# Performance work log

Measured on AMD Instinct MI355X. Metric: run time of the kernel, lower is better.

## Reference

```python
import jax, jax.numpy as jnp
import numpy as np

B, S, D = 4, 2048, 1024


def setup_inputs() -> dict:
    key = jax.random.key(0)
    ks = jax.random.split(key, 7)
    s = 1.0 / np.sqrt(D)
    return {
        "x": jax.random.normal(ks[0], (B, S, D), dtype=jnp.float32),
        "Wq": jax.random.normal(ks[1], (D, D), dtype=jnp.float32) * s,
        "bq": jnp.zeros((D,), dtype=jnp.float32),
        "Wk": jax.random.normal(ks[2], (D, D), dtype=jnp.float32) * s,
        "bk": jnp.zeros((D,), dtype=jnp.float32),
        "Wv": jax.random.normal(ks[3], (D, D), dtype=jnp.float32) * s,
        "bv": jnp.zeros((D,), dtype=jnp.float32),
    }


def reference(x, Wq, bq, Wk, bk, Wv, bv):
    # Linear layers: x @ W^T + b (torch nn.Linear convention)
    Q = jnp.einsum("bsd,ed->bse", x, Wq) + bq
    K = jnp.einsum("bsd,ed->bse", x, Wk) + bk
    V = jnp.einsum("bsd,ed->bse", x, Wv) + bv
    scale = 1.0 / (x.shape[-1] ** 0.5)
    scores = jnp.einsum("bse,bte->bst", Q, K) * scale  # [B, S, S]
    attn = jax.nn.softmax(scores, axis=-1)
    out = jnp.einsum("bst,bte->bse", attn, V)
    return out
```

## Files before the change

kernel.cpp:

```cpp
#include <hip/hip_runtime.h>
#include <math.h>


typedef _Float16 f16;
typedef _Float16 f16x8 __attribute__((ext_vector_type(8)));
typedef _Float16 f16x4 __attribute__((ext_vector_type(4)));
typedef float f32x4 __attribute__((ext_vector_type(4)));

__device__ __forceinline__ void glds16(const void* g, const void* l) {
    __builtin_amdgcn_global_load_lds(
        (const __attribute__((address_space(1))) void*)g,
        (__attribute__((address_space(3))) void*)l, 16, 0, 0);
}

__global__ __launch_bounds__(256) void cvt16_kernel(
    const float* __restrict__ in, f16* __restrict__ o, int n4)
{
    int i = blockIdx.x * 256 + threadIdx.x;
    if (i >= n4) return;
    float4 v = ((const float4*)in)[i];
    f16x4 h = { (f16)v.x, (f16)v.y, (f16)v.z, (f16)v.w };
    ((f16x4*)o)[i] = h;
}

__global__ __launch_bounds__(256) void cvtw_kernel(
    const float* __restrict__ Wq, const float* __restrict__ Wk,
    const float* __restrict__ Wv, f16* __restrict__ o, int n4)
{
    int i = blockIdx.x * 256 + threadIdx.x;
    if (i >= n4) return;
    const float* src = (blockIdx.y == 0) ? Wq : (blockIdx.y == 1) ? Wk : Wv;
    float4 v = ((const float4*)src)[i];
    f16x4 h = { (f16)v.x, (f16)v.y, (f16)v.z, (f16)v.w };
    ((f16x4*)(o + (size_t)blockIdx.y * 1024 * 1024))[i] = h;
}

__global__ __launch_bounds__(256) void zero_kernel(float* __restrict__ p, int n)
{
    int i = blockIdx.x * 256 + threadIdx.x;
    if (i < n) p[i] = 0.0f;
}

__device__ __forceinline__ void mfma_core(
    const f16* __restrict__ A, int lda,
    const f16* __restrict__ B, int ldb,
    int K, int m0, int n0, f16* sm, f32x4 acc[4][4])
{
    f16* sA = sm;
    f16* sB = sm + 8192;

    const int tid  = threadIdx.x;
    const int lane = tid & 63;
    const int wave = tid >> 6;
    const int wm = (wave >> 1) * 64;
    const int wn = (wave & 1) * 64;
    const int lr = lane & 15;
    const int kq = lane >> 4;

    const int srow  = wave * 32;
    const int rloc  = lane >> 3;
    const int chunk = (lane & 7) ^ rloc;
    const int gcol  = chunk * 8;

    const f16* gA = A + (size_t)(m0 + srow + rloc) * lda + gcol;
    const f16* gB = B + (size_t)(n0 + srow + rloc) * ldb + gcol;

    f16* lA = sA + srow * 64;
    f16* lB = sB + srow * 64;

    for (int k0 = 0; k0 < K; k0 += 64) {
        #pragma unroll
        for (int p = 0; p < 4; ++p) {
            glds16(gA + k0 + (size_t)(p * 8) * lda, lA + p * 512);
            glds16(gB + k0 + (size_t)(p * 8) * ldb, lB + p * 512);
        }
        __syncthreads();

        #pragma unroll
        for (int kk = 0; kk < 2; ++kk) {
            f16x8 a[4], b[4];
            #pragma unroll
            for (int i = 0; i < 4; ++i) {
                const int ra = wm + i * 16 + lr;
                const int rb = wn + i * 16 + lr;
                const int c  = kk * 4 + kq;
                a[i] = *(const f16x8*)&sA[ra * 64 + ((c ^ (ra & 7)) * 8)];
                b[i] = *(const f16x8*)&sB[rb * 64 + ((c ^ (rb & 7)) * 8)];
            }
            #pragma unroll
            for (int i = 0; i < 4; ++i)
                #pragma unroll
                for (int j = 0; j < 4; ++j)
                    acc[i][j] = __builtin_amdgcn_mfma_f32_16x16x32_f16(a[i], b[j], acc[i][j], 0, 0, 0);
        }
        __syncthreads();
    }
}

__global__ __launch_bounds__(256) void qkv_mfma_kernel(
    const f16* __restrict__ xh, const f16* __restrict__ Wh,
    const float* __restrict__ bq, const float* __restrict__ bk,
    const float* __restrict__ bv,
    f16* __restrict__ Qh, f16* __restrict__ Kh, f16* __restrict__ Vh)
{
    __shared__ __align__(16) f16 smem[16384];
    const int z  = blockIdx.z;
    const int m0 = blockIdx.y * 128;
    const int n0 = blockIdx.x * 128;

    f32x4 acc[4][4];
    #pragma unroll
    for (int i = 0; i < 4; ++i)
        #pragma unroll
        for (int j = 0; j < 4; ++j) acc[i][j] = (f32x4){0.f, 0.f, 0.f, 0.f};

    mfma_core(xh, 1024, Wh + (size_t)z * 1024 * 1024, 1024, 1024, m0, n0, smem, acc);

    const float* bias = (z == 0) ? bq : (z == 1) ? bk : bv;
    const float  sc   = (z == 0) ? 0.03125f : 1.0f;
    f16* C = (z == 0) ? Qh : (z == 1) ? Kh : Vh;
    const int lane = threadIdx.x & 63;
    const int wave = threadIdx.x >> 6;
    const int wm = (wave >> 1) * 64;
    const int wn = (wave & 1) * 64;
    const int col  = lane & 15;
    const int quad = lane >> 4;

    #pragma unroll
    for (int j = 0; j < 4; ++j) {
        const int gn = n0 + wn + j * 16 + col;
        const float bb = bias[gn];
        #pragma unroll
        for (int i = 0; i < 4; ++i)
            #pragma unroll
            for (int r = 0; r < 4; ++r) {
                const int gm = m0 + wm + i * 16 + quad * 4 + r;
                C[(size_t)gm * 1024 + gn] = (f16)((acc[i][j][r] + bb) * sc);
            }
    }
}

__global__ __launch_bounds__(256) void vtrans_kernel(
    const f16* __restrict__ V, f16* __restrict__ Vt)
{
    __shared__ f16 t[64][72];
    const int b  = blockIdx.z;
    const int s0 = blockIdx.x * 64;
    const int d0 = blockIdx.y * 64;
    const int tid = threadIdx.x;

    const int r  = tid >> 3;
    const int c8 = (tid & 7) * 8;
    const f16* src = V + ((size_t)b * 2048 + s0) * 1024 + d0;
    *(f16x8*)&t[r][c8]      = *(const f16x8*)(src + (size_t)r * 1024 + c8);
    *(f16x8*)&t[r + 32][c8] = *(const f16x8*)(src + (size_t)(r + 32) * 1024 + c8);
    __syncthreads();

    const int dl  = tid >> 2;
    const int sl0 = (tid & 3) * 16;
    f16* dst = Vt + ((size_t)b * 1024 + d0 + dl) * 2048 + s0 + sl0;
    f16 buf[16];
    #pragma unroll
    for (int u = 0; u < 16; ++u) buf[u] = t[sl0 + u][dl];
    *(f16x8*)dst       = *(f16x8*)&buf[0];
    *(f16x8*)(dst + 8) = *(f16x8*)&buf[8];
}

__global__ __launch_bounds__(256) void scores_exp_kernel(
    const f16* __restrict__ Qh, const f16* __restrict__ Kh,
    f16* __restrict__ P, float* __restrict__ sums)
{
    __shared__ __align__(16) f16 smem[16384];
    const int b  = blockIdx.z;
    const int m0 = blockIdx.y * 128;
    const int n0 = blockIdx.x * 128;

    f32x4 acc[4][4];
    #pragma unroll
    for (int i = 0; i < 4; ++i)
        #pragma unroll
        for (int j = 0; j < 4; ++j) acc[i][j] = (f32x4){0.f, 0.f, 0.f, 0.f};

    const size_t ao = (size_t)b * 2048 * 1024;
    mfma_core(Qh + ao, 1024, Kh + ao, 1024, 1024, m0, n0, smem, acc);

    const int lane = threadIdx.x & 63;
    const int wave = threadIdx.x >> 6;
    const int wm = (wave >> 1) * 64;
    const int wn = (wave & 1) * 64;
    const int col  = lane & 15;
    const int quad = lane >> 4;
    f16* C = P + (size_t)b * 2048 * 2048;

    float rp[4][4];
    #pragma unroll
    for (int i = 0; i < 4; ++i)
        #pragma unroll
        for (int r = 0; r < 4; ++r) rp[i][r] = 0.0f;

    #pragma unroll
    for (int i = 0; i < 4; ++i)
        #pragma unroll
        for (int r = 0; r < 4; ++r) {
            const int gm = m0 + wm + i * 16 + quad * 4 + r;
            #pragma unroll
            for (int j = 0; j < 4; ++j) {
                const int gn = n0 + wn + j * 16 + col;
                const f16 p = (f16)__expf(acc[i][j][r]);
                C[(size_t)gm * 2048 + gn] = p;
                rp[i][r] += (float)p;
            }
        }

    #pragma unroll
    for (int i = 0; i < 4; ++i)
        #pragma unroll
        for (int r = 0; r < 4; ++r) {
            float v = rp[i][r];
            v += __shfl_xor(v, 1);
            v += __shfl_xor(v, 2);
            v += __shfl_xor(v, 4);
            v += __shfl_xor(v, 8);
            rp[i][r] = v;
        }
    if (col == 0) {
        #pragma unroll
        for (int i = 0; i < 4; ++i)
            #pragma unroll
            for (int r = 0; r < 4; ++r) {
                const int row = m0 + wm + i * 16 + quad * 4 + r;
                atomicAdd(&sums[b * 2048 + row], rp[i][r]);
            }
    }
}

__global__ __launch_bounds__(256) void pv_mfma_kernel(
    const f16* __restrict__ P, const f16* __restrict__ Vt,
    const float* __restrict__ sums, float* __restrict__ out)
{
    __shared__ __align__(16) f16 smem[16384];
    const int b  = blockIdx.z;
    const int m0 = blockIdx.y * 128;
    const int n0 = blockIdx.x * 128;

    f32x4 acc[4][4];
    #pragma unroll
    for (int i = 0; i < 4; ++i)
        #pragma unroll
        for (int j = 0; j < 4; ++j) acc[i][j] = (f32x4){0.f, 0.f, 0.f, 0.f};

    const size_t ao = (size_t)b * 2048 * 2048;
    const size_t bo = (size_t)b * 1024 * 2048;
    mfma_core(P + ao, 2048, Vt + bo, 2048, 2048, m0, n0, smem, acc);

    const int lane = threadIdx.x & 63;
    const int wave = threadIdx.x >> 6;
    const int wm = (wave >> 1) * 64;
    const int wn = (wave & 1) * 64;
    const int col  = lane & 15;
    const int quad = lane >> 4;
    float* C = out + (size_t)b * 2048 * 1024;

    #pragma unroll
    for (int i = 0; i < 4; ++i)
        #pragma unroll
        for (int r = 0; r < 4; ++r) {
            const int rl = m0 + wm + i * 16 + quad * 4 + r;
            const float inv = 1.0f / sums[b * 2048 + rl];
            #pragma unroll
            for (int j = 0; j < 4; ++j) {
                const int gn = n0 + wn + j * 16 + col;
                C[(size_t)rl * 1024 + gn] = acc[i][j][r] * inv;
            }
        }
}

extern "C" void kernel_launch(void* const* d_in, const int* in_sizes, int n_in,
                              void* d_out, int out_size, void* d_ws, size_t ws_size,
                              hipStream_t stream)
{
    (void)in_sizes; (void)n_in; (void)out_size; (void)ws_size;
    const int Bn = 4, S = 2048, D = 1024;
    const float* x  = (const float*)d_in[0];
    const float* Wq = (const float*)d_in[1];
    const float* bq = (const float*)d_in[2];
    const float* Wk = (const float*)d_in[3];
    const float* bk = (const float*)d_in[4];
    const float* Wv = (const float*)d_in[5];
    const float* bv = (const float*)d_in[6];
    float* out = (float*)d_out;

    const size_t MB = 1024 * 1024;
    char* w = (char*)d_ws;
    f16*   xh   = (f16*)(w + 0 * MB);
    f16*   Wh3  = (f16*)(w + 16 * MB);
    f16*   Vh   = (f16*)(w + 22 * MB);
    f16*   Qh   = (f16*)(w + 38 * MB);
    f16*   Kh   = (f16*)(w + 54 * MB);
    f16*   Vt   = (f16*)(w + 70 * MB);
    float* sums = (float*)(w + 86 * MB);
    f16*   P    = (f16*)(w + 0 * MB);

    cvt16_kernel<<<dim3(Bn * S * D / 4 / 256), 256, 0, stream>>>(x, xh, Bn * S * D / 4);
    cvtw_kernel<<<dim3(D * D / 4 / 256, 3), 256, 0, stream>>>(Wq, Wk, Wv, Wh3, D * D / 4);
    zero_kernel<<<dim3((Bn * S + 255) / 256), 256, 0, stream>>>(sums, Bn * S);

    qkv_mfma_kernel<<<dim3(D / 128, (Bn * S) / 128, 3), 256, 0, stream>>>(
        xh, Wh3, bq, bk, bv, Qh, Kh, Vh);
    vtrans_kernel<<<dim3(S / 64, D / 64, Bn), 256, 0, stream>>>(Vh, Vt);

    scores_exp_kernel<<<dim3(S / 128, S / 128, Bn), 256, 0, stream>>>(
        Qh, Kh, P, sums);
    pv_mfma_kernel<<<dim3(D / 128, S / 128, Bn), 256, 0, stream>>>(
        P, Vt, sums, out);
}
```

Baseline: 272.3 us.

## Triple-buffer GEMM core with 256x128 tiles, 8 waves, and grid swizzle

Replaces the single-buffered shared-memory GEMM mainloop with a three-stage async global-to-LDS pipeline using explicit vmcnt waits and raw barriers, so tile loads overlap MFMA work. Block tiles grow to 256x128 with 512 threads (8 waves), using 144KB of dynamic LDS, and the QKV projection grid is remapped with a block-index swizzle to improve cache locality. Adds setprio around the MFMA bursts. Risks lower occupancy from the large LDS footprint and fragile hand-tuned waitcnt counts.

```diff
diff --git a/kernel.cpp b/kernel.cpp
--- a/kernel.cpp
+++ b/kernel.cpp
@@ -41,72 +41,110 @@
     if (i < n) p[i] = 0.0f;
 }
 
-__device__ __forceinline__ void mfma_core(
+#define ABUF 16384
+#define BBUF 8192
+#define BOFF 49152
+
+__device__ __forceinline__ void mfma_core3(
     const f16* __restrict__ A, int lda,
     const f16* __restrict__ B, int ldb,
     int K, int m0, int n0, f16* sm, f32x4 acc[4][4])
 {
-    f16* sA = sm;
-    f16* sB = sm + 8192;
-
     const int tid  = threadIdx.x;
     const int lane = tid & 63;
-    const int wave = tid >> 6;
-    const int wm = (wave >> 1) * 64;
-    const int wn = (wave & 1) * 64;
-    const int lr = lane & 15;
-    const int kq = lane >> 4;
-
-    const int srow  = wave * 32;
-    const int rloc  = lane >> 3;
-    const int chunk = (lane & 7) ^ rloc;
-    const int gcol  = chunk * 8;
-
-    const f16* gA = A + (size_t)(m0 + srow + rloc) * lda + gcol;
-    const f16* gB = B + (size_t)(n0 + srow + rloc) * ldb + gcol;
-
-    f16* lA = sA + srow * 64;
-    f16* lB = sB + srow * 64;
-
-    for (int k0 = 0; k0 < K; k0 += 64) {
-        #pragma unroll
-        for (int p = 0; p < 4; ++p) {
-            glds16(gA + k0 + (size_t)(p * 8) * lda, lA + p * 512);
-            glds16(gB + k0 + (size_t)(p * 8) * ldb, lB + p * 512);
-        }
-        __syncthreads();
-
+    const int w    = tid >> 6;
+    const int wr   = w >> 1;
+    const int wc   = w & 1;
+    const int lr   = lane & 15;
+    const int kq   = lane >> 4;
+
+    const int rl = lane >> 3;
+    const int ch = (lane & 7) ^ rl;
+
+    const f16* gA[4];
+    #pragma unroll
+    for (int p = 0; p < 4; ++p)
+        gA[p] = A + (size_t)(m0 + p * 64 + w * 8 + rl) * lda + ch * 8;
+    const f16* gB[2];
+    #pragma unroll
+    for (int p = 0; p < 2; ++p)
+        gB[p] = B + (size_t)(n0 + p * 64 + w * 8 + rl) * ldb + ch * 8;
+
+    const int NT = K >> 6;
+
+    #pragma unroll
+    for (int s = 0; s < 2; ++s) {
+        f16* lA = sm + s * ABUF + w * 8 * 64;
+        f16* lB = sm + BOFF + s * BBUF + w * 8 * 64;
+        #pragma unroll
+        for (int p = 0; p < 4; ++p) glds16(gA[p] + s * 64, lA + p * 4096);
+        #pragma unroll
+        for (int p = 0; p < 2; ++p) glds16(gB[p] + s * 64, lB + p * 4096);
+    }
+
+    int kst = 128, sb = 2, cur = 0;
+    for (int t = 0; t < NT; ++t) {
+        if (t + 2 < NT) {
+            f16* lA = sm + sb * ABUF + w * 8 * 64;
+            f16* lB = sm + BOFF + sb * BBUF + w * 8 * 64;
+            #pragma unroll
+            for (int p = 0; p < 4; ++p) glds16(gA[p] + kst, lA + p * 4096);
+            #pragma unroll
+            for (int p = 0; p < 2; ++p) glds16(gB[p] + kst, lB + p * 4096);
+            kst += 64;
+            sb = (sb == 2) ? 0 : sb + 1;
+        }
+        if (t + 2 < NT)      asm volatile("s_waitcnt vmcnt(12)" ::: "memory");
+        else if (t + 1 < NT) asm volatile("s_waitcnt vmcnt(6)"  ::: "memory");
+        else                 asm volatile("s_waitcnt vmcnt(0)"  ::: "memory");
+        asm volatile("s_barrier" ::: "memory");
+
+        const f16* sA = sm + cur * ABUF;
+        const f16* sB = sm + BOFF + cur * BBUF;
         #pragma unroll
         for (int kk = 0; kk < 2; ++kk) {
             f16x8 a[4], b[4];
+            const int c = kk * 4 + kq;
             #pragma unroll
             for (int i = 0; i < 4; ++i) {
-                const int ra = wm + i * 16 + lr;
-                const int rb = wn + i * 16 + lr;
-                const int c  = kk * 4 + kq;
-                a[i] = *(const f16x8*)&sA[ra * 64 + ((c ^ (ra & 7)) * 8)];
-                b[i] = *(const f16x8*)&sB[rb * 64 + ((c ^ (rb & 7)) * 8)];
-            }
+                const int ar = wr * 64 + i * 16 + lr;
+                a[i] = *(const f16x8*)&sA[ar * 64 + ((c ^ (ar & 7)) * 8)];
+            }
+            #pragma unroll
+            for (int j = 0; j < 4; ++j) {
+                const int br = wc * 64 + j * 16 + lr;
+                b[j] = *(const f16x8*)&sB[br * 64 + ((c ^ (br & 7)) * 8)];
+            }
+            asm volatile("s_waitcnt lgkmcnt(0)" ::: "memory");
+            __builtin_amdgcn_sched_barrier(0);
+            __builtin_amdgcn_s_setprio(1);
             #pragma unroll
             for (int i = 0; i < 4; ++i)
                 #pragma unroll
                 for (int j = 0; j < 4; ++j)
                     acc[i][j] = __builtin_amdgcn_mfma_f32_16x16x32_f16(a[i], b[j], acc[i][j], 0, 0, 0);
-        }
-        __syncthreads();
-    }
-}
-
-__global__ __launch_bounds__(256) void qkv_mfma_kernel(
+            __builtin_amdgcn_s_setprio(0);
+            asm volatile("s_barrier" ::: "memory");
+        }
+        cur = (cur == 2) ? 0 : cur + 1;
+    }
+}
+
+__global__ __launch_bounds__(512) void qkv_mfma_kernel(
     const f16* __restrict__ xh, const f16* __restrict__ Wh,
     const float* __restrict__ bq, const float* __restrict__ bk,
     const float* __restrict__ bv,
     f16* __restrict__ Qh, f16* __restrict__ Kh, f16* __restrict__ Vh)
 {
-    __shared__ __align__(16) f16 smem[16384];
-    const int z  = blockIdx.z;
-    const int m0 = blockIdx.y * 128;
-    const int n0 = blockIdx.x * 128;
+    extern __shared__ __align__(16) f16 smem[];
+    int flat = blockIdx.x + 8 * (blockIdx.y + 32 * blockIdx.z);
+    flat = (flat & 7) * 96 + (flat >> 3);
+    const int bx = flat & 7;
+    const int by = (flat >> 3) & 31;
+    const int bz = flat >> 8;
+
+    const int m0 = by * 256;
+    const int n0 = bx * 128;
 
     f32x4 acc[4][4];
     #pragma unroll
@@ -114,27 +152,26 @@
         #pragma unroll
         for (int j = 0; j < 4; ++j) acc[i][j] = (f32x4){0.f, 0.f, 0.f, 0.f};
 
-    mfma_core(xh, 1024, Wh + (size_t)z * 1024 * 1024, 1024, 1024, m0, n0, smem, acc);
-
-    const float* bias = (z == 0) ? bq : (z == 1) ? bk : bv;
-    const float  sc   = (z == 0) ? 0.03125f : 1.0f;
-    f16* C = (z == 0) ? Qh : (z == 1) ? Kh : Vh;
+    mfma_core3(xh, 1024, Wh + (size_t)bz * 1024 * 1024, 1024, 1024, m0, n0, smem, acc);
+
+    const float* bias = (bz == 0) ? bq : (bz == 1) ? bk : bv;
+    const float  sc   = (bz == 0) ? 0.03125f : 1.0f;
+    f16* C = (bz == 0) ? Qh : (bz == 1) ? Kh : Vh;
     const int lane = threadIdx.x & 63;
-    const int wave = threadIdx.x >> 6;
-    const int wm = (wave >> 1) * 64;
-    const int wn = (wave & 1) * 64;
+    const int w    = threadIdx.x >> 6;
+    const int wr = w >> 1, wc = w & 1;
     const int col  = lane & 15;
     const int quad = lane >> 4;
 
     #pragma unroll
     for (int j = 0; j < 4; ++j) {
-        const int gn = n0 + wn + j * 16 + col;
+        const int gn = n0 + wc * 64 + j * 16 + col;
         const float bb = bias[gn];
         #pragma unroll
         for (int i = 0; i < 4; ++i)
             #pragma unroll
             for (int r = 0; r < 4; ++r) {
-                const int gm = m0 + wm + i * 16 + quad * 4 + r;
+                const int gm = m0 + wr * 64 + i * 16 + quad * 4 + r;
                 C[(size_t)gm * 1024 + gn] = (f16)((acc[i][j][r] + bb) * sc);
             }
     }
@@ -166,13 +203,13 @@
     *(f16x8*)(dst + 8) = *(f16x8*)&buf[8];
 }
 
-__global__ __launch_bounds__(256) void scores_exp_kernel(
+__global__ __launch_bounds__(512) void scores_exp_kernel(
     const f16* __restrict__ Qh, const f16* __restrict__ Kh,
     f16* __restrict__ P, float* __restrict__ sums)
 {
-    __shared__ __align__(16) f16 smem[16384];
+    extern __shared__ __align__(16) f16 smem[];
     const int b  = blockIdx.z;
-    const int m0 = blockIdx.y * 128;
+    const int m0 = blockIdx.y * 256;
     const int n0 = blockIdx.x * 128;
 
     f32x4 acc[4][4];
@@ -182,12 +219,11 @@
         for (int j = 0; j < 4; ++j) acc[i][j] = (f32x4){0.f, 0.f, 0.f, 0.f};
 
     const size_t ao = (size_t)b * 2048 * 1024;
-    mfma_core(Qh + ao, 1024, Kh + ao, 1024, 1024, m0, n0, smem, acc);
+    mfma_core3(Qh + ao, 1024, Kh + ao, 1024, 1024, m0, n0, smem, acc);
 
     const int lane = threadIdx.x & 63;
-    const int wave = threadIdx.x >> 6;
-    const int wm = (wave >> 1) * 64;
-    const int wn = (wave & 1) * 64;
+    const int w    = threadIdx.x >> 6;
+    const int wr = w >> 1, wc = w & 1;
     const int col  = lane & 15;
     const int quad = lane >> 4;
     f16* C = P + (size_t)b * 2048 * 2048;
@@ -202,10 +238,10 @@
     for (int i = 0; i < 4; ++i)
         #pragma unroll
         for (int r = 0; r < 4; ++r) {
-            const int gm = m0 + wm + i * 16 + quad * 4 + r;
+            const int gm = m0 + wr * 64 + i * 16 + quad * 4 + r;
             #pragma unroll
             for (int j = 0; j < 4; ++j) {
-                const int gn = n0 + wn + j * 16 + col;
+                const int gn = n0 + wc * 64 + j * 16 + col;
                 const f16 p = (f16)__expf(acc[i][j][r]);
                 C[(size_t)gm * 2048 + gn] = p;
                 rp[i][r] += (float)p;
@@ -228,19 +264,19 @@
         for (int i = 0; i < 4; ++i)
             #pragma unroll
             for (int r = 0; r < 4; ++r) {
-                const int row = m0 + wm + i * 16 + quad * 4 + r;
+                const int row = m0 + wr * 64 + i * 16 + quad * 4 + r;
                 atomicAdd(&sums[b * 2048 + row], rp[i][r]);
             }
     }
 }
 
-__global__ __launch_bounds__(256) void pv_mfma_kernel(
+__global__ __launch_bounds__(512) void pv_mfma_kernel(
     const f16* __restrict__ P, const f16* __restrict__ Vt,
     const float* __restrict__ sums, float* __restrict__ out)
 {
-    __shared__ __align__(16) f16 smem[16384];
+    extern __shared__ __align__(16) f16 smem[];
     const int b  = blockIdx.z;
-    const int m0 = blockIdx.y * 128;
+    const int m0 = blockIdx.y * 256;
     const int n0 = blockIdx.x * 128;
 
     f32x4 acc[4][4];
@@ -251,12 +287,11 @@
 
     const size_t ao = (size_t)b * 2048 * 2048;
     const size_t bo = (size_t)b * 1024 * 2048;
-    mfma_core(P + ao, 2048, Vt + bo, 2048, 2048, m0, n0, smem, acc);
+    mfma_core3(P + ao, 2048, Vt + bo, 2048, 2048, m0, n0, smem, acc);
 
     const int lane = threadIdx.x & 63;
-    const int wave = threadIdx.x >> 6;
-    const int wm = (wave >> 1) * 64;
-    const int wn = (wave & 1) * 64;
+    const int w    = threadIdx.x >> 6;
+    const int wr = w >> 1, wc = w & 1;
     const int col  = lane & 15;
     const int quad = lane >> 4;
     float* C = out + (size_t)b * 2048 * 1024;
@@ -265,12 +300,12 @@
     for (int i = 0; i < 4; ++i)
         #pragma unroll
         for (int r = 0; r < 4; ++r) {
-            const int rl = m0 + wm + i * 16 + quad * 4 + r;
-            const float inv = 1.0f / sums[b * 2048 + rl];
+            const int rowg = m0 + wr * 64 + i * 16 + quad * 4 + r;
+            const float inv = 1.0f / sums[b * 2048 + rowg];
             #pragma unroll
             for (int j = 0; j < 4; ++j) {
-                const int gn = n0 + wn + j * 16 + col;
-                C[(size_t)rl * 1024 + gn] = acc[i][j][r] * inv;
+                const int gn = n0 + wc * 64 + j * 16 + col;
+                C[(size_t)rowg * 1024 + gn] = acc[i][j][r] * inv;
             }
         }
 }
@@ -301,16 +336,27 @@
     float* sums = (float*)(w + 86 * MB);
     f16*   P    = (f16*)(w + 0 * MB);
 
+    static bool attr_set = false;
+    if (!attr_set) {
+        hipFuncSetAttribute(reinterpret_cast<const void*>(qkv_mfma_kernel),
+                            hipFuncAttributeMaxDynamicSharedMemorySize, 147456);
+        hipFuncSetAttribute(reinterpret_cast<const void*>(scores_exp_kernel),
+                            hipFuncAttributeMaxDynamicSharedMemorySize, 147456);
+        hipFuncSetAttribute(reinterpret_cast<const void*>(pv_mfma_kernel),
+                            hipFuncAttributeMaxDynamicSharedMemorySize, 147456);
+        attr_set = true;
+    }
+
     cvt16_kernel<<<dim3(Bn * S * D / 4 / 256), 256, 0, stream>>>(x, xh, Bn * S * D / 4);
     cvtw_kernel<<<dim3(D * D / 4 / 256, 3), 256, 0, stream>>>(Wq, Wk, Wv, Wh3, D * D / 4);
     zero_kernel<<<dim3((Bn * S + 255) / 256), 256, 0, stream>>>(sums, Bn * S);
 
-    qkv_mfma_kernel<<<dim3(D / 128, (Bn * S) / 128, 3), 256, 0, stream>>>(
+    qkv_mfma_kernel<<<dim3(D / 128, (Bn * S) / 256, 3), 512, 147456, stream>>>(
         xh, Wh3, bq, bk, bv, Qh, Kh, Vh);
     vtrans_kernel<<<dim3(S / 64, D / 64, Bn), 256, 0, stream>>>(Vh, Vt);
 
-    scores_exp_kernel<<<dim3(S / 128, S / 128, Bn), 256, 0, stream>>>(
+    scores_exp_kernel<<<dim3(S / 128, S / 256, Bn), 512, 147456, stream>>>(
         Qh, Kh, P, sums);
-    pv_mfma_kernel<<<dim3(D / 128, S / 128, Bn), 256, 0, stream>>>(
+    pv_mfma_kernel<<<dim3(D / 128, S / 256, Bn), 512, 147456, stream>>>(
         P, Vt, sums, out);
 }
```

Result: no change. 267.1 us (-1.9%).
